# Kernel optimization log

Measured on AMD Instinct MI355X. Metric: run time of the kernel, lower is better.

Reference implementation:

```python
import jax, jax.numpy as jnp
import numpy as np

B, N, D = 8, 8192, 512
H, WIDTH = 8, 2048
DH = D // H
EPS = 1e-5


def _ln(x, g, b):
    m = jnp.mean(x, axis=-1, keepdims=True)
    v = jnp.mean(jnp.square(x - m), axis=-1, keepdims=True)
    return (x - m) * jax.lax.rsqrt(v + EPS) * g + b


def setup_inputs() -> dict:
    key = jax.random.key(0)
    ks = jax.random.split(key, 16)
    s = 0.02
    return {
        "x": jax.random.normal(ks[0], (B, N, D), dtype=jnp.float32),
        "mask": jnp.ones((B, N), dtype=jnp.float32),
        "Wq": jax.random.normal(ks[1], (D, D), dtype=jnp.float32) * s,
        "bq": jnp.zeros((D,), dtype=jnp.float32),
        "Wk": jax.random.normal(ks[2], (D, D), dtype=jnp.float32) * s,
        "bk": jnp.zeros((D,), dtype=jnp.float32),
        "Wv": jax.random.normal(ks[3], (D, D), dtype=jnp.float32) * s,
        "bv": jnp.zeros((D,), dtype=jnp.float32),
        "q_alpha": jax.random.normal(ks[4], (H, DH), dtype=jnp.float32),
        "k_beta": jax.random.normal(ks[5], (H, DH), dtype=jnp.float32),
        "Wo": jax.random.normal(ks[6], (D, D), dtype=jnp.float32) * s,
        "bo": jnp.zeros((D,), dtype=jnp.float32),
        "ln0_g": jnp.ones((D,), dtype=jnp.float32),
        "ln0_b": jnp.zeros((D,), dtype=jnp.float32),
        "ln1_g": jnp.ones((D,), dtype=jnp.float32),
        "ln1_b": jnp.zeros((D,), dtype=jnp.float32),
        "W1": jax.random.normal(ks[7], (WIDTH, D), dtype=jnp.float32) * s,
        "b1": jnp.zeros((WIDTH,), dtype=jnp.float32),
        "W2": jax.random.normal(ks[8], (D, WIDTH), dtype=jnp.float32) * s,
        "b2": jnp.zeros((D,), dtype=jnp.float32),
    }


def reference(x, mask, Wq, bq, Wk, bk, Wv, bv, q_alpha, k_beta, Wo, bo,
              ln0_g, ln0_b, ln1_g, ln1_b, W1, b1, W2, b2):
    scale = DH ** -0.5
    mask_ = mask[..., None]                       # [B,N,1]
    valid = (mask != 0)[..., None]                # [B,N,1] bool, broadcast over H

    residual = x
    xn = _ln(x, ln0_g, ln0_b) * mask_

    Q = (xn @ Wq.T + bq).reshape(B, N, H, DH)
    K = (xn @ Wk.T + bk).reshape(B, N, H, DH)
    V = (xn @ Wv.T + bv).reshape(B, N, H, DH)

    # stage 1: global query pooling
    alpha = jnp.einsum('bnhd,hd->bnh', Q, q_alpha) * scale
    alpha = jnp.where(valid, alpha, -jnp.inf)
    alpha = jax.nn.softmax(alpha, axis=1)         # softmax over N
    global_q = jnp.einsum('bnhd,bnh->bhd', Q, alpha)

    # stage 2: global value pooling
    P = K * global_q[:, None]                     # [B,N,H,DH]
    beta = jnp.einsum('bnhd,hd->bnh', P, k_beta) * scale
    beta = jnp.where(valid, beta, -jnp.inf)
    beta = jax.nn.softmax(beta, axis=1)
    global_v = jnp.einsum('bnhd,bnh->bhd', V, beta)

    out = (Q + global_v[:, None]).reshape(B, N, D)
    out = out @ Wo.T + bo
    x = residual + out

    residual = x
    xn = _ln(x, ln1_g, ln1_b)
    h = jax.nn.gelu(xn @ W1.T + b1, approximate=False)
    h = jax.nn.gelu(h @ W2.T + b2, approximate=False)
    x = residual + h
    x = x * mask_
    return x
```

## Files before the change

### kernel.cpp

```cpp
#include <hip/hip_runtime.h>
#include <hip/hip_bf16.h>
#include <hip/hip_fp8.h>
#include <math.h>

typedef short s8v __attribute__((ext_vector_type(8)));
typedef short s4v __attribute__((ext_vector_type(4)));
typedef __bf16 bf8v __attribute__((ext_vector_type(8)));
typedef float f4v __attribute__((ext_vector_type(4)));

#define GLOBAL_AS __attribute__((address_space(1)))
#define LDS_AS __attribute__((address_space(3)))

static __device__ __forceinline__ float bf2f(ushort u) {
  return __builtin_bit_cast(float, (unsigned int)u << 16);
}
static __device__ __forceinline__ ushort f2bf(float f) {
  unsigned int u = __builtin_bit_cast(unsigned int, f);
  u += 0x7FFFu + ((u >> 16) & 1u);
  return (ushort)(u >> 16);
}
static __device__ __forceinline__ unsigned char f2fp8(float f) {
#if __has_builtin(__builtin_amdgcn_cvt_pk_fp8_f32)
  int p = __builtin_amdgcn_cvt_pk_fp8_f32(f, f, 0, false);
  return (unsigned char)(p & 0xFF);
#else
  __hip_fp8_e4m3 v(f);
  return (unsigned char)v.__x;
#endif
}
static __device__ __forceinline__ float gelu_f(float v) {
  float t = v * v;
  float u = v * (0.0356774081f * t + 0.7978845608f);
  float e = __expf(-2.0f * u);
  return v * __builtin_amdgcn_rcpf(1.0f + e);
}
static __device__ __forceinline__ float wave_max_f(float v) {
  #pragma unroll
  for (int o = 32; o >= 1; o >>= 1) v = fmaxf(v, __shfl_xor(v, o));
  return v;
}
static __device__ __forceinline__ float wave_sum_f(float v) {
  #pragma unroll
  for (int o = 32; o >= 1; o >>= 1) v += __shfl_xor(v, o);
  return v;
}
static __device__ __forceinline__ void gload16(const void* g, const void* l) {
  __builtin_amdgcn_global_load_lds(
      (const GLOBAL_AS unsigned int*)g,
      (LDS_AS unsigned int*)l, 16, 0, 0);
}

__global__ void cvt_f32_bf16(const float* __restrict__ in, ushort* __restrict__ out, int n) {
  int i = (blockIdx.x * 256 + threadIdx.x) * 4;
  if (i >= n) return;
  float4 v = *(const float4*)(in + i);
  s4v o;
  o[0] = (short)f2bf(v.x); o[1] = (short)f2bf(v.y);
  o[2] = (short)f2bf(v.z); o[3] = (short)f2bf(v.w);
  *(s4v*)(out + i) = o;
}

__global__ void cvt_f32_fp8(const float* __restrict__ in, unsigned char* __restrict__ out, int n) {
  int i = (blockIdx.x * 256 + threadIdx.x) * 4;
  if (i >= n) return;
  float4 v = *(const float4*)(in + i);
  uchar4 o;
  o.x = f2fp8(v.x); o.y = f2fp8(v.y); o.z = f2fp8(v.z); o.w = f2fp8(v.w);
  *(uchar4*)(out + i) = o;
}

__global__ __launch_bounds__(256) void transpose512(
    const float* __restrict__ in, float* __restrict__ out) {
  __shared__ float t[32][33];
  const int bx = blockIdx.x & 15, by = blockIdx.x >> 4;
  const int tx = threadIdx.x & 31, ty = threadIdx.x >> 5;
  #pragma unroll
  for (int i = 0; i < 4; ++i)
    t[ty + i * 8][tx] = in[(long)(by * 32 + ty + i * 8) * 512 + bx * 32 + tx];
  __syncthreads();
  #pragma unroll
  for (int i = 0; i < 4; ++i)
    out[(long)(bx * 32 + ty + i * 8) * 512 + by * 32 + tx] = t[tx][ty + i * 8];
}

__global__ __launch_bounds__(256) void wqo_kernel(
    const float* __restrict__ Wo, const float* __restrict__ Wq,
    ushort* __restrict__ WqoB)
{
  __shared__ float lO[64][33];
  __shared__ float lQ[32][65];
  const int t = threadIdx.x;
  const int bi = (blockIdx.x & 7) * 64, bj = (blockIdx.x >> 3) * 64;
  float acc[16] = {};
  for (int k0 = 0; k0 < 512; k0 += 32) {
    __syncthreads();
    {
      const int r = t >> 2, c = (t & 3) * 8;
      #pragma unroll
      for (int j = 0; j < 8; ++j) lO[r][c + j] = Wo[(long)(bi + r) * 512 + k0 + c + j];
      const int r2 = t >> 3, c2 = (t & 7) * 8;
      #pragma unroll
      for (int j = 0; j < 8; ++j) lQ[r2][c2 + j] = Wq[(long)(k0 + r2) * 512 + bj + c2 + j];
    }
    __syncthreads();
    const int j = t & 63, ig = t >> 6;
    for (int kk = 0; kk < 32; ++kk) {
      float q = lQ[kk][j];
      #pragma unroll
      for (int ii = 0; ii < 16; ++ii) acc[ii] += lO[ig * 16 + ii][kk] * q;
    }
  }
  const int j = t & 63, ig = t >> 6;
  #pragma unroll
  for (int ii = 0; ii < 16; ++ii)
    WqoB[(long)(bi + ig * 16 + ii) * 512 + bj + j] = f2bf(acc[ii]);
}

__global__ __launch_bounds__(256) void wa_kernel(
    const float* __restrict__ qa, const float* __restrict__ Wq,
    const float* __restrict__ bqv, ushort* __restrict__ waB, float* __restrict__ ca)
{
  __shared__ float ql[64];
  const int h = blockIdx.x;
  const int t = threadIdx.x;
  if (h >= 8) {
    waB[h * 512 + t] = 0; waB[h * 512 + 256 + t] = 0;
    if (t == 0) ca[h] = 0.f;
    return;
  }
  if (t < 64) ql[t] = qa[h * 64 + t];
  __syncthreads();
  #pragma unroll
  for (int half = 0; half < 2; ++half) {
    const int k = half * 256 + t;
    float s = 0;
    for (int dd = 0; dd < 64; ++dd) s += ql[dd] * Wq[(long)(h * 64 + dd) * 512 + k];
    waB[h * 512 + k] = f2bf(s);
  }
  if (t == 0) {
    float s = 0;
    for (int dd = 0; dd < 64; ++dd) s += ql[dd] * bqv[h * 64 + dd];
    ca[h] = s;
  }
}

__global__ __launch_bounds__(256) void ln_rows(
    const float* __restrict__ x, const float* __restrict__ gam,
    const float* __restrict__ bet, const float* __restrict__ mask,
    ushort* __restrict__ out)
{
  const int tid = threadIdx.x, lane = tid & 63, wv = tid >> 6;
  const long row = (long)blockIdx.x * 4 + wv;
  const float* xp = x + row * 512 + lane * 8;
  float4 a = *(const float4*)xp;
  float4 b = *(const float4*)(xp + 4);
  float s = a.x + a.y + a.z + a.w + b.x + b.y + b.z + b.w;
  float q = a.x*a.x + a.y*a.y + a.z*a.z + a.w*a.w
          + b.x*b.x + b.y*b.y + b.z*b.z + b.w*b.w;
  s = wave_sum_f(s); q = wave_sum_f(q);
  float m = s * (1.f / 512.f);
  float var = q * (1.f / 512.f) - m * m;
  float r = rsqrtf(var + 1e-5f);
  float mk = mask ? mask[row] : 1.f;
  const float* gp = gam + lane * 8;
  const float* bp = bet + lane * 8;
  float4 g0 = *(const float4*)gp, g1 = *(const float4*)(gp + 4);
  float4 c0 = *(const float4*)bp, c1 = *(const float4*)(bp + 4);
  s8v o;
  o[0] = (short)f2bf(((a.x - m) * r * g0.x + c0.x) * mk);
  o[1] = (short)f2bf(((a.y - m) * r * g0.y + c0.y) * mk);
  o[2] = (short)f2bf(((a.z - m) * r * g0.z + c0.z) * mk);
  o[3] = (short)f2bf(((a.w - m) * r * g0.w + c0.w) * mk);
  o[4] = (short)f2bf(((b.x - m) * r * g1.x + c1.x) * mk);
  o[5] = (short)f2bf(((b.y - m) * r * g1.y + c1.y) * mk);
  o[6] = (short)f2bf(((b.z - m) * r * g1.z + c1.z) * mk);
  o[7] = (short)f2bf(((b.w - m) * r * g1.w + c1.w) * mk);
  *(s8v*)(out + row * 512 + lane * 8) = o;
}

__global__ __launch_bounds__(256) void ln_rows_bf16(
    const ushort* __restrict__ x, const float* __restrict__ gam,
    const float* __restrict__ bet, ushort* __restrict__ out)
{
  const int tid = threadIdx.x, lane = tid & 63, wv = tid >> 6;
  const long row = (long)blockIdx.x * 4 + wv;
  s8v v = *(const s8v*)(x + row * 512 + lane * 8);
  float xv[8];
  #pragma unroll
  for (int j = 0; j < 8; ++j) xv[j] = bf2f((ushort)v[j]);
  float s = 0.f, q = 0.f;
  #pragma unroll
  for (int j = 0; j < 8; ++j) { s += xv[j]; q += xv[j] * xv[j]; }
  s = wave_sum_f(s); q = wave_sum_f(q);
  float m = s * (1.f / 512.f);
  float var = q * (1.f / 512.f) - m * m;
  float r = rsqrtf(var + 1e-5f);
  const float* gp = gam + lane * 8;
  const float* bp = bet + lane * 8;
  float4 g0 = *(const float4*)gp, g1 = *(const float4*)(gp + 4);
  float4 c0 = *(const float4*)bp, c1 = *(const float4*)(bp + 4);
  float gg[8] = {g0.x, g0.y, g0.z, g0.w, g1.x, g1.y, g1.z, g1.w};
  float cc[8] = {c0.x, c0.y, c0.z, c0.w, c1.x, c1.y, c1.z, c1.w};
  s8v o;
  #pragma unroll
  for (int j = 0; j < 8; ++j) o[j] = (short)f2bf((xv[j] - m) * r * gg[j] + cc[j]);
  *(s8v*)(out + row * 512 + lane * 8) = o;
}

template<int BS, int CS>
__global__ __launch_bounds__(256) void logits_k(
    const ushort* __restrict__ XN, const ushort* __restrict__ Wl,
    const float* __restrict__ cvec, const float* __restrict__ mask,
    float* __restrict__ outL)
{
  __shared__ ushort lw[16 * 512];
  const int tid = threadIdx.x, lane = tid & 63, wv = tid >> 6;
  const long r0 = (long)blockIdx.x * 64;
  const int b = (int)(r0 >> 13);
  #pragma unroll
  for (int i = 0; i < 4; ++i) {
    const int u = tid + i * 256;
    const int h2 = u >> 6, uu = u & 63;
    s8v v = *(const s8v*)(Wl + (long)b * BS + h2 * 512 + uu * 8);
    *(s8v*)(lw + h2 * 512 + (uu ^ (h2 & 7)) * 8) = v;
  }
  __syncthreads();
  const int h = lane & 15, q = lane >> 4;
  const long rw = r0 + wv * 16;
  const ushort* ap = XN + (rw + (lane & 15)) * 512 + q * 8;
  f4v acc = {};
  #pragma unroll
  for (int t = 0; t < 16; ++t) {
    bf8v a = *(const bf8v*)(ap + t * 32);
    bf8v bb = *(const bf8v*)(lw + h * 512 + (((t * 4 + q) ^ (h & 7))) * 8);
    acc = __builtin_amdgcn_mfma_f32_16x16x32_bf16(a, bb, acc, 0, 0, 0);
  }
  const float cv = cvec[b * CS + h];
  #pragma unroll
  for (int j = 0; j < 4; ++j) {
    const long n = rw + q * 4 + j;
    float v = (acc[j] + cv) * 0.125f;
    if (mask[n] == 0.f) v = -1e30f;
    if (h < 8) outL[((long)((b << 3) + h) << 13) + (n & 8191)] = v;
  }
}

__global__ __launch_bounds__(1024) void softmax_rows(float* __restrict__ L)
{
  __shared__ float red[16];
  __shared__ float bc;
  const int tid = threadIdx.x, lane = tid & 63, wv = tid >> 6;
  float* p = L + ((long)blockIdx.x << 13) + tid * 8;
  float4 v0 = *(float4*)p;
  float4 v1 = *(float4*)(p + 4);
  float m = fmaxf(fmaxf(fmaxf(v0.x, v0.y), fmaxf(v0.z, v0.w)),
                  fmaxf(fmaxf(v1.x, v1.y), fmaxf(v1.z, v1.w)));
  m = wave_max_f(m);
  if (lane == 0) red[wv] = m;
  __syncthreads();
  if (tid < 64) {
    float t = (lane < 16) ? red[lane] : -INFINITY;
    t = wave_max_f(t);
    if (lane == 0) bc = t;
  }
  __syncthreads();
  const float gm = bc;
  v0.x = __expf(v0.x - gm); v0.y = __expf(v0.y - gm);
  v0.z = __expf(v0.z - gm); v0.w = __expf(v0.w - gm);
  v1.x = __expf(v1.x - gm); v1.y = __expf(v1.y - gm);
  v1.z = __expf(v1.z - gm); v1.w = __expf(v1.w - gm);
  float s = v0.x + v0.y + v0.z + v0.w + v1.x + v1.y + v1.z + v1.w;
  s = wave_sum_f(s);
  __syncthreads();
  if (lane == 0) red[wv] = s;
  __syncthreads();
  if (tid < 64) {
    float t = (lane < 16) ? red[lane] : 0.f;
    t = wave_sum_f(t);
    if (lane == 0) bc = t;
  }
  __syncthreads();
  const float inv = 1.0f / bc;
  v0.x *= inv; v0.y *= inv; v0.z *= inv; v0.w *= inv;
  v1.x *= inv; v1.y *= inv; v1.z *= inv; v1.w *= inv;
  *(float4*)p = v0;
  *(float4*)(p + 4) = v1;
}

__global__ __launch_bounds__(256) void pool_w(
    const ushort* __restrict__ XN, const float* __restrict__ wbuf,
    float* __restrict__ part)
{
  __shared__ float wlds[128][8];
  __shared__ float cmb[4][512];
  const int tid = threadIdx.x;
  const int b = blockIdx.x >> 6, ch = blockIdx.x & 63;
  const long g0 = ((long)b << 13) + ch * 128;
  if (tid < 128) {
    #pragma unroll
    for (int h = 0; h < 8; ++h)
      wlds[tid][h] = wbuf[(((long)(b * 8 + h)) << 13) + ch * 128 + tid];
  }
  __syncthreads();
  const int rg = tid >> 6, c8 = (tid & 63) * 8;
  f4v acc[8][2] = {};
  for (int it = 0; it < 32; ++it) {
    const int r = it * 4 + rg;
    s8v xv = *(const s8v*)(XN + (g0 + r) * 512 + c8);
    float xf[8];
    #pragma unroll
    for (int j = 0; j < 8; ++j) xf[j] = bf2f((ushort)xv[j]);
    #pragma unroll
    for (int h = 0; h < 8; ++h) {
      const float w = wlds[r][h];
      #pragma unroll
      for (int j = 0; j < 8; ++j) acc[h][j >> 2][j & 3] += w * xf[j];
    }
  }
  #pragma unroll
  for (int h = 0; h < 8; ++h) {
    __syncthreads();
    #pragma unroll
    for (int j = 0; j < 8; ++j) cmb[rg][c8 + j] = acc[h][j >> 2][j & 3];
    __syncthreads();
    const int col = tid * 2;
    float s0 = cmb[0][col] + cmb[1][col] + cmb[2][col] + cmb[3][col];
    float s1 = cmb[0][col + 1] + cmb[1][col + 1] + cmb[2][col + 1] + cmb[3][col + 1];
    *(float2*)(part + (((long)blockIdx.x * 8 + h) << 9) + col) = make_float2(s0, s1);
  }
}

__global__ __launch_bounds__(256) void combine_px(
    const float* __restrict__ part, float* __restrict__ px)
{
  const int bh = blockIdx.x;
  const int b = bh >> 3, h = bh & 7;
  const int col = threadIdx.x * 2;
  float s0 = 0.f, s1 = 0.f;
  for (int ch = 0; ch < 64; ++ch) {
    const float* p = part + (((long)((b * 64 + ch) * 8 + h)) << 9) + col;
    s0 += p[0]; s1 += p[1];
  }
  px[(bh << 9) + col] = s0;
  px[(bh << 9) + col + 1] = s1;
}

__global__ __launch_bounds__(64) void prep_gq_wb(
    const float* __restrict__ px, const float* __restrict__ WqT,
    const float* __restrict__ bqv, const float* __restrict__ kbv,
    const float* __restrict__ Wk, const float* __restrict__ bkv,
    ushort* __restrict__ wbB, float* __restrict__ cbs)
{
  __shared__ float pxl[512];
  __shared__ float gkb[64];
  const int bh = blockIdx.x, b = bh >> 3, h = bh & 7, d = threadIdx.x;
  #pragma unroll
  for (int i = 0; i < 8; ++i) pxl[d + i * 64] = px[(bh << 9) + d + i * 64];
  __syncthreads();
  float acc = bqv[h * 64 + d];
  for (int c = 0; c < 512; ++c) acc += pxl[c] * WqT[(long)c * 512 + h * 64 + d];
  gkb[d] = acc * kbv[h * 64 + d];
  __syncthreads();
  float s[8] = {};
  for (int dd = 0; dd < 64; ++dd) {
    const float g = gkb[dd];
    const float* wr = Wk + (long)(h * 64 + dd) * 512 + d;
    #pragma unroll
    for (int ki = 0; ki < 8; ++ki) s[ki] += g * wr[ki * 64];
  }
  #pragma unroll
  for (int ki = 0; ki < 8; ++ki)
    wbB[(long)(b * 16 + h) * 512 + d + ki * 64] = f2bf(s[ki]);
  if (d == 0) {
    float t = 0.f;
    for (int dd = 0; dd < 64; ++dd) t += gkb[dd] * bkv[h * 64 + dd];
    cbs[b * 16 + h] = t;
  }
  if (h == 0) {
    #pragma unroll
    for (int hp = 8; hp < 16; ++hp)
      for (int k = d; k < 512; k += 64) wbB[(long)(b * 16 + hp) * 512 + k] = 0;
    if (d < 8) cbs[b * 16 + 8 + d] = 0.f;
  }
}

__global__ __launch_bounds__(64) void prep_gv(
    const float* __restrict__ pv, const float* __restrict__ WvT,
    const float* __restrict__ bvv, const float* __restrict__ bqv,
    float* __restrict__ gvb)
{
  __shared__ float pxl[512];
  const int bh = blockIdx.x, b = bh >> 3, h = bh & 7, d = threadIdx.x;
  #pragma unroll
  for (int i = 0; i < 8; ++i) pxl[d + i * 64] = pv[(bh << 9) + d + i * 64];
  __syncthreads();
  float acc = bvv[h * 64 + d] + bqv[h * 64 + d];
  for (int c = 0; c < 512; ++c) acc += pxl[c] * WvT[(long)c * 512 + h * 64 + d];
  gvb[b * 512 + h * 64 + d] = acc;
}

__global__ __launch_bounds__(256) void bias_gv(
    const float* __restrict__ gv, const float* __restrict__ Wo,
    const float* __restrict__ bo, float* __restrict__ bo2) {
  const int b = blockIdx.x;
  const int n = blockIdx.y * 256 + threadIdx.x;
  const float* g = gv + b * 512;
  const float* w = Wo + (long)n * 512;
  float acc = 0.f;
  for (int d = 0; d < 512; d += 4) {
    float4 wv4 = *(const float4*)(w + d);
    acc += g[d] * wv4.x + g[d + 1] * wv4.y + g[d + 2] * wv4.z + g[d + 3] * wv4.w;
  }
  bo2[b * 512 + n] = bo[n] + acc;
}

#define MFMA_(d,a,b) d = __builtin_amdgcn_mfma_f32_16x16x32_bf16(a, b, d, 0, 0, 0)

template<int EPI, int LDA, int NN, int KK>
__global__ __launch_bounds__(512, 4) void gemmP(
    const ushort* __restrict__ A, const ushort* __restrict__ W,
    const float* __restrict__ bias, const void* __restrict__ resid,
    const float* __restrict__ mask, void* __restrict__ Out)
{
  constexpr int NBX = NN / 256;
  constexpr int NT = KK / 32;
  __shared__ __align__(16) ushort lds[3][12288];
  const int tid = threadIdx.x;
  const int lane = tid & 63;
  const int w = tid >> 6;
  const int wm = w >> 2, wn = w & 3;

  const int nwg = gridDim.x;
  const int cpx = nwg >> 3;
  const int wg = (blockIdx.x & 7) * cpx + (blockIdx.x >> 3);
  const int bx = wg % NBX, by = wg / NBX;
  const long bm = (long)by * 128;
  const int bn = bx * 256;

  const int scr = tid >> 2, sls = tid & 3;
  const int akU = ((sls ^ (scr & 3) ^ ((scr >> 2) & 3))) * 8;
  const ushort* asrc = A + (bm + scr) * (long)LDA + akU;
  const int rbe = (scr & 31) + ((scr >> 5) << 6);
  const ushort* besrc = W + (long)(bn + rbe) * KK + akU;
  const ushort* bosrc = W + (long)(bn + rbe + 32) * KK + akU;

#define STG(b_, Tt) { \
    gload16(asrc + (Tt) * 32, &lds[b_][tid * 8]); \
    gload16(besrc + (Tt) * 32, &lds[b_][4096 + tid * 8]); \
    gload16(bosrc + (Tt) * 32, &lds[b_][8192 + tid * 8]); }

  STG(0, 0);
  STG(1, 1);

  f4v acc[4][4] = {};

  const int L = lane & 15, q = lane >> 4;
  const int soff = (q ^ (lane & 3) ^ ((lane >> 2) & 3)) * 8;
  const int abase = (wm * 64 + L) * 32 + soff;
  const int bbase = 4096 + (wn * 32 + L) * 32 + soff;

  asm volatile("s_waitcnt vmcnt(3)" ::: "memory");
  asm volatile("s_barrier" ::: "memory");

  for (int T = 0; T < NT; ++T) {
    const ushort* Lp = &lds[T % 3][0];
    bf8v aR[4], bR[4];
    #pragma unroll
    for (int m = 0; m < 4; ++m) aR[m] = *(const bf8v*)(Lp + abase + m * 512);
    bR[0] = *(const bf8v*)(Lp + bbase);
    bR[1] = *(const bf8v*)(Lp + bbase + 512);
    bR[2] = *(const bf8v*)(Lp + bbase + 4096);
    bR[3] = *(const bf8v*)(Lp + bbase + 4096 + 512);
    if (T + 2 < NT) {
      STG((T + 2) % 3, T + 2);
      asm volatile("s_waitcnt vmcnt(3)" ::: "memory");
    } else {
      asm volatile("s_waitcnt vmcnt(0)" ::: "memory");
    }
    asm volatile("s_barrier" ::: "memory");
    __builtin_amdgcn_s_setprio(1);
    #pragma unroll
    for (int m = 0; m < 4; ++m)
      #pragma unroll
      for (int n = 0; n < 4; ++n)
        MFMA_(acc[m][n], aR[m], bR[n]);
    __builtin_amdgcn_s_setprio(0);
  }
#undef STG

  const int colb = bn + wn * 64 + L;
  const long rowb = bm + wm * 64 + q * 4;
  const float* biasp = (EPI == 5) ? bias + ((bm >> 13) << 9) : bias;
  #pragma unroll
  for (int m = 0; m < 4; ++m) {
    #pragma unroll
    for (int j = 0; j < 4; ++j) {
      const long row = rowb + m * 16 + j;
      #pragma unroll
      for (int n = 0; n < 4; ++n) {
        const int col = colb + n * 16;
        float v = acc[m][n][j] + biasp[col];
        const long idx = row * (long)NN + col;
        if constexpr (EPI == 6) {
          ((unsigned char*)Out)[idx] = f2fp8(gelu_f(v));
        } else {
          ((ushort*)Out)[idx] = f2bf(v + ((const float*)resid)[idx]);
        }
      }
    }
  }
}

__global__ __launch_bounds__(512, 4) void gemmF8(
    const unsigned char* __restrict__ A, const unsigned char* __restrict__ W,
    const float* __restrict__ bias, const ushort* __restrict__ resid,
    const float* __restrict__ mask, float* __restrict__ Out)
{
  constexpr int NN = 512, KK = 2048;
  constexpr int NBX = 2;
  constexpr int NT = KK / 64;
  __shared__ __align__(16) unsigned char lds8[3][24576];
  const int tid = threadIdx.x;
  const int lane = tid & 63;
  const int w = tid >> 6;
  const int wm = w >> 2, wn = w & 3;

  const int nwg = gridDim.x;
  const int cpx = nwg >> 3;
  const int wg = (blockIdx.x & 7) * cpx + (blockIdx.x >> 3);
  const int bx = wg % NBX, by = wg / NBX;
  const long bm = (long)by * 128;
  const int bn = bx * 256;

  const int srow = tid >> 2;
  const int sxu = (tid & 3) ^ ((srow >> 1) & 3);
  const unsigned char* asrc = A + (bm + srow) * (long)KK + sxu * 16;
  const unsigned char* b0src = W + (long)(bn + srow) * KK + sxu * 16;
  const unsigned char* b1src = W + (long)(bn + srow + 128) * KK + sxu * 16;

#define STG8(b_, Tt) { \
    gload16(asrc + (Tt) * 64, &lds8[b_][tid * 16]); \
    gload16(b0src + (Tt) * 64, &lds8[b_][8192 + tid * 16]); \
    gload16(b1src + (Tt) * 64, &lds8[b_][16384 + tid * 16]); }

  STG8(0, 0);
  STG8(1, 1);

  f4v acc[4][4] = {};

  const int L = lane & 15, q = lane >> 4;
  const int s0 = ((q) ^ (L & 6)) * 8;
  const int s1 = ((4 + q) ^ (L & 6)) * 8;
  const int arow = (wm * 64 + L) * 64;
  const int brow = 8192 + (wn * 64 + L) * 64;

  asm volatile("s_waitcnt vmcnt(3)" ::: "memory");
  asm volatile("s_barrier" ::: "memory");

  for (int T = 0; T < NT; ++T) {
    const unsigned char* Lp = &lds8[T % 3][0];
    long aF[8], bF[8];
    #pragma unroll
    for (int m = 0; m < 4; ++m) {
      aF[2 * m]     = *(const long*)(Lp + arow + m * 1024 + s0);
      aF[2 * m + 1] = *(const long*)(Lp + arow + m * 1024 + s1);
    }
    #pragma unroll
    for (int n = 0; n < 4; ++n) {
      bF[2 * n]     = *(const long*)(Lp + brow + n * 1024 + s0);
      bF[2 * n + 1] = *(const long*)(Lp + brow + n * 1024 + s1);
    }
    if (T + 2 < NT) {
      STG8((T + 2) % 3, T + 2);
      asm volatile("s_waitcnt vmcnt(3)" ::: "memory");
    } else {
      asm volatile("s_waitcnt vmcnt(0)" ::: "memory");
    }
    asm volatile("s_barrier" ::: "memory");
    __builtin_amdgcn_s_setprio(1);
    #pragma unroll
    for (int m = 0; m < 4; ++m)
      #pragma unroll
      for (int n = 0; n < 4; ++n) {
        acc[m][n] = __builtin_amdgcn_mfma_f32_16x16x32_fp8_fp8(
            aF[2 * m], bF[2 * n], acc[m][n], 0, 0, 0);
        acc[m][n] = __builtin_amdgcn_mfma_f32_16x16x32_fp8_fp8(
            aF[2 * m + 1], bF[2 * n + 1], acc[m][n], 0, 0, 0);
      }
    __builtin_amdgcn_s_setprio(0);
  }
#undef STG8

  const int colb = bn + wn * 64 + L;
  const long rowb = bm + wm * 64 + q * 4;
  #pragma unroll
  for (int m = 0; m < 4; ++m) {
    #pragma unroll
    for (int j = 0; j < 4; ++j) {
      const long row = rowb + m * 16 + j;
      const float mk = mask[row];
      #pragma unroll
      for (int n = 0; n < 4; ++n) {
        const int col = colb + n * 16;
        float v = acc[m][n][j] + bias[col];
        const long idx = row * (long)NN + col;
        Out[idx] = (bf2f(resid[idx]) + gelu_f(v)) * mk;
      }
    }
  }
}

extern "C" void kernel_launch(void* const* d_in, const int* in_sizes, int n_in,
                              void* d_out, int out_size, void* d_ws, size_t ws_size,
                              hipStream_t stream) {
  const float* x    = (const float*)d_in[0];
  const float* mask = (const float*)d_in[1];
  const float* Wq   = (const float*)d_in[2];
  const float* bq   = (const float*)d_in[3];
  const float* Wk   = (const float*)d_in[4];
  const float* bk   = (const float*)d_in[5];
  const float* Wv   = (const float*)d_in[6];
  const float* bv   = (const float*)d_in[7];
  const float* qa   = (const float*)d_in[8];
  const float* kb   = (const float*)d_in[9];
  const float* Wo   = (const float*)d_in[10];
  const float* bo   = (const float*)d_in[11];
  const float* g0   = (const float*)d_in[12];
  const float* be0  = (const float*)d_in[13];
  const float* g1   = (const float*)d_in[14];
  const float* be1  = (const float*)d_in[15];
  const float* W1   = (const float*)d_in[16];
  const float* b1   = (const float*)d_in[17];
  const float* W2   = (const float*)d_in[18];
  const float* b2   = (const float*)d_in[19];
  float* out = (float*)d_out;

  const int M = 65536;
  char* ws = (char*)d_ws;
  const size_t MB = 1024 * 1024;
  ushort* XN  = (ushort*)(ws);
  ushort* X1  = (ushort*)(ws + 64 * MB);
  unsigned char* H1F = (unsigned char*)(ws + 192 * MB);
  float*  AL  = (float*)(ws + 192 * MB);
  float*  BL  = (float*)(ws + 194 * MB);
  float*  PART= (float*)(ws + 196 * MB);
  char* base = ws + 448 * MB;
  ushort* W1B  = (ushort*)(base);
  unsigned char* W2F = (unsigned char*)(base + 2 * MB);
  ushort* WqoB = (ushort*)(base + 4 * MB);
  float*  WqT  = (float*)(base + 4 * MB + 512 * 1024);
  float*  WvT  = (float*)(base + 5 * MB + 512 * 1024);
  ushort* waB  = (ushort*)(base + 6 * MB + 512 * 1024);
  ushort* wbB  = (ushort*)(base + 6 * MB + 528 * 1024);
  float*  ca   = (float*)(base + 6 * MB + 656 * 1024);
  float*  cbs  = (float*)(base + 6 * MB + 660 * 1024);
  float*  PX   = (float*)(base + 6 * MB + 664 * 1024);
  float*  PV   = (float*)(base + 6 * MB + 792 * 1024);
  float*  GVB  = (float*)(base + 6 * MB + 920 * 1024);
  float*  BO2  = (float*)(base + 6 * MB + 936 * 1024);

  cvt_f32_bf16<<<1024, 256, 0, stream>>>(W1, W1B, 1048576);
  cvt_f32_fp8<<<1024, 256, 0, stream>>>(W2, W2F, 1048576);
  wqo_kernel<<<64, 256, 0, stream>>>(Wo, Wq, WqoB);
  wa_kernel<<<16, 256, 0, stream>>>(qa, Wq, bq, waB, ca);
  transpose512<<<256, 256, 0, stream>>>(Wq, WqT);
  transpose512<<<256, 256, 0, stream>>>(Wv, WvT);

  ln_rows<<<M / 4, 256, 0, stream>>>(x, g0, be0, mask, XN);

  logits_k<0, 0><<<1024, 256, 0, stream>>>(XN, waB, ca, mask, AL);
  softmax_rows<<<64, 1024, 0, stream>>>(AL);
  pool_w<<<512, 256, 0, stream>>>(XN, AL, PART);
  combine_px<<<64, 256, 0, stream>>>(PART, PX);
  prep_gq_wb<<<64, 64, 0, stream>>>(PX, WqT, bq, kb, Wk, bk, wbB, cbs);

  logits_k<8192, 16><<<1024, 256, 0, stream>>>(XN, wbB, cbs, mask, BL);
  softmax_rows<<<64, 1024, 0, stream>>>(BL);
  pool_w<<<512, 256, 0, stream>>>(XN, BL, PART);
  combine_px<<<64, 256, 0, stream>>>(PART, PV);
  prep_gv<<<64, 64, 0, stream>>>(PV, WvT, bv, bq, GVB);
  bias_gv<<<dim3(8, 2), 256, 0, stream>>>(GVB, Wo, bo, BO2);

  gemmP<5, 512, 512, 512><<<2 * (M / 128), 512, 0, stream>>>(
      XN, WqoB, BO2, x, nullptr, X1);

  ln_rows_bf16<<<M / 4, 256, 0, stream>>>(X1, g1, be1, XN);

  gemmP<6, 512, 2048, 512><<<8 * (M / 128), 512, 0, stream>>>(
      XN, W1B, b1, nullptr, nullptr, H1F);
  gemmF8<<<2 * (M / 128), 512, 0, stream>>>(
      H1F, W2F, b2, X1, mask, out);
}
```

Baseline: 631.8 us.

## Run FFN first GEMM in FP8 with interleaved K layout and 16-byte fragment loads

Moves the W1 GEMM from bf16 to FP8. LN1 now writes FP8 activations and the weights are pre-scaled by 8 and stored in a K-interleaved layout, so each lane fetches both MFMA operands with a single 16-byte LDS read. The shared FP8 GEMM is templated for both FFN matmuls, drops from triple to double buffering with an extra barrier, and the first GEMM's epilogue writes GELU outputs in the same interleaved FP8 layout. This halves A/B traffic and doubles MFMA throughput for the first GEMM, at the cost of lower precision from FP8 activations after LN.

```diff
diff --git a/kernel.cpp b/kernel.cpp
--- a/kernel.cpp
+++ b/kernel.cpp
@@ -7,6 +7,7 @@
 typedef short s4v __attribute__((ext_vector_type(4)));
 typedef __bf16 bf8v __attribute__((ext_vector_type(8)));
 typedef float f4v __attribute__((ext_vector_type(4)));
+typedef long l2v __attribute__((ext_vector_type(2)));
 
 #define GLOBAL_AS __attribute__((address_space(1)))
 #define LDS_AS __attribute__((address_space(3)))
@@ -50,23 +51,19 @@
       (LDS_AS unsigned int*)l, 16, 0, 0);
 }
 
-__global__ void cvt_f32_bf16(const float* __restrict__ in, ushort* __restrict__ out, int n) {
+__global__ void cvt_f32_fp8il(const float* __restrict__ in,
+                              unsigned char* __restrict__ out, int n, int kmask) {
   int i = (blockIdx.x * 256 + threadIdx.x) * 4;
   if (i >= n) return;
   float4 v = *(const float4*)(in + i);
-  s4v o;
-  o[0] = (short)f2bf(v.x); o[1] = (short)f2bf(v.y);
-  o[2] = (short)f2bf(v.z); o[3] = (short)f2bf(v.w);
-  *(s4v*)(out + i) = o;
-}
-
-__global__ void cvt_f32_fp8(const float* __restrict__ in, unsigned char* __restrict__ out, int n) {
-  int i = (blockIdx.x * 256 + threadIdx.x) * 4;
-  if (i >= n) return;
-  float4 v = *(const float4*)(in + i);
-  uchar4 o;
-  o.x = f2fp8(v.x); o.y = f2fp8(v.y); o.z = f2fp8(v.z); o.w = f2fp8(v.w);
-  *(uchar4*)(out + i) = o;
+  const int k = i & kmask;
+  const int r = k & 63;
+  const int qq = (r >> 3) & 3, h = (r >> 5) & 1, j = r & 7;
+  const long o = (long)(i - r) + qq * 16 + h * 8 + j;
+  uchar4 ob;
+  ob.x = f2fp8(v.x * 8.f); ob.y = f2fp8(v.y * 8.f);
+  ob.z = f2fp8(v.z * 8.f); ob.w = f2fp8(v.w * 8.f);
+  *(uchar4*)(out + o) = ob;
 }
 
 __global__ __launch_bounds__(256) void transpose512(
@@ -178,9 +175,9 @@
   *(s8v*)(out + row * 512 + lane * 8) = o;
 }
 
-__global__ __launch_bounds__(256) void ln_rows_bf16(
+__global__ __launch_bounds__(256) void ln_rows_fp8il(
     const ushort* __restrict__ x, const float* __restrict__ gam,
-    const float* __restrict__ bet, ushort* __restrict__ out)
+    const float* __restrict__ bet, unsigned char* __restrict__ out)
 {
   const int tid = threadIdx.x, lane = tid & 63, wv = tid >> 6;
   const long row = (long)blockIdx.x * 4 + wv;
@@ -201,10 +198,14 @@
   float4 c0 = *(const float4*)bp, c1 = *(const float4*)(bp + 4);
   float gg[8] = {g0.x, g0.y, g0.z, g0.w, g1.x, g1.y, g1.z, g1.w};
   float cc[8] = {c0.x, c0.y, c0.z, c0.w, c1.x, c1.y, c1.z, c1.w};
-  s8v o;
-  #pragma unroll
-  for (int j = 0; j < 8; ++j) o[j] = (short)f2bf((xv[j] - m) * r * gg[j] + cc[j]);
-  *(s8v*)(out + row * 512 + lane * 8) = o;
+  unsigned long long pk = 0;
+  #pragma unroll
+  for (int j = 0; j < 8; ++j) {
+    unsigned char b8 = f2fp8((xv[j] - m) * r * gg[j] + cc[j]);
+    pk |= (unsigned long long)b8 << (8 * j);
+  }
+  *(unsigned long long*)(out + row * 512 + (lane >> 3) * 64
+                         + (lane & 3) * 16 + ((lane >> 2) & 1) * 8) = pk;
 }
 
 template<int BS, int CS>
@@ -490,7 +491,7 @@
 
   const int colb = bn + wn * 64 + L;
   const long rowb = bm + wm * 64 + q * 4;
-  const float* biasp = (EPI == 5) ? bias + ((bm >> 13) << 9) : bias;
+  const float* biasp = bias + ((bm >> 13) << 9);
   #pragma unroll
   for (int m = 0; m < 4; ++m) {
     #pragma unroll
@@ -501,25 +502,21 @@
         const int col = colb + n * 16;
         float v = acc[m][n][j] + biasp[col];
         const long idx = row * (long)NN + col;
-        if constexpr (EPI == 6) {
-          ((unsigned char*)Out)[idx] = f2fp8(gelu_f(v));
-        } else {
-          ((ushort*)Out)[idx] = f2bf(v + ((const float*)resid)[idx]);
-        }
+        ((ushort*)Out)[idx] = f2bf(v + ((const float*)resid)[idx]);
       }
     }
   }
 }
 
+template<int EPI, int NN, int KK>
 __global__ __launch_bounds__(512, 4) void gemmF8(
     const unsigned char* __restrict__ A, const unsigned char* __restrict__ W,
-    const float* __restrict__ bias, const ushort* __restrict__ resid,
-    const float* __restrict__ mask, float* __restrict__ Out)
-{
-  constexpr int NN = 512, KK = 2048;
-  constexpr int NBX = 2;
+    const float* __restrict__ bias, const void* __restrict__ resid,
+    const float* __restrict__ mask, void* __restrict__ Out)
+{
+  constexpr int NBX = NN / 256;
   constexpr int NT = KK / 64;
-  __shared__ __align__(16) unsigned char lds8[3][24576];
+  __shared__ __align__(16) unsigned char lds8[2][24576];
   const int tid = threadIdx.x;
   const int lane = tid & 63;
   const int w = tid >> 6;
@@ -533,15 +530,15 @@
   const int bn = bx * 256;
 
   const int srow = tid >> 2;
-  const int sxu = (tid & 3) ^ ((srow >> 1) & 3);
-  const unsigned char* asrc = A + (bm + srow) * (long)KK + sxu * 16;
-  const unsigned char* b0src = W + (long)(bn + srow) * KK + sxu * 16;
-  const unsigned char* b1src = W + (long)(bn + srow + 128) * KK + sxu * 16;
-
-#define STG8(b_, Tt) { \
-    gload16(asrc + (Tt) * 64, &lds8[b_][tid * 16]); \
-    gload16(b0src + (Tt) * 64, &lds8[b_][8192 + tid * 16]); \
-    gload16(b1src + (Tt) * 64, &lds8[b_][16384 + tid * 16]); }
+  const int sgu = (tid & 3) ^ ((srow >> 1) & 3);
+  const unsigned char* asrc = A + (bm + srow) * (long)KK + sgu * 16;
+  const unsigned char* b0src = W + (long)(bn + srow) * KK + sgu * 16;
+  const unsigned char* b1src = W + (long)(bn + 128 + srow) * KK + sgu * 16;
+
+#define STG8(bf_, Tt) { \
+    gload16(asrc + (Tt) * 64, &lds8[bf_][tid * 16]); \
+    gload16(b0src + (Tt) * 64, &lds8[bf_][8192 + tid * 16]); \
+    gload16(b1src + (Tt) * 64, &lds8[bf_][16384 + tid * 16]); }
 
   STG8(0, 0);
   STG8(1, 1);
@@ -549,8 +546,7 @@
   f4v acc[4][4] = {};
 
   const int L = lane & 15, q = lane >> 4;
-  const int s0 = ((q) ^ (L & 6)) * 8;
-  const int s1 = ((4 + q) ^ (L & 6)) * 8;
+  const int ua = (q ^ ((L >> 1) & 3)) * 16;
   const int arow = (wm * 64 + L) * 64;
   const int brow = 8192 + (wn * 64 + L) * 64;
 
@@ -558,20 +554,15 @@
   asm volatile("s_barrier" ::: "memory");
 
   for (int T = 0; T < NT; ++T) {
-    const unsigned char* Lp = &lds8[T % 3][0];
-    long aF[8], bF[8];
-    #pragma unroll
-    for (int m = 0; m < 4; ++m) {
-      aF[2 * m]     = *(const long*)(Lp + arow + m * 1024 + s0);
-      aF[2 * m + 1] = *(const long*)(Lp + arow + m * 1024 + s1);
-    }
-    #pragma unroll
-    for (int n = 0; n < 4; ++n) {
-      bF[2 * n]     = *(const long*)(Lp + brow + n * 1024 + s0);
-      bF[2 * n + 1] = *(const long*)(Lp + brow + n * 1024 + s1);
-    }
+    const unsigned char* Lp = &lds8[T & 1][0];
+    l2v aV[4], bV[4];
+    #pragma unroll
+    for (int m = 0; m < 4; ++m) aV[m] = *(const l2v*)(Lp + arow + m * 1024 + ua);
+    #pragma unroll
+    for (int n = 0; n < 4; ++n) bV[n] = *(const l2v*)(Lp + brow + n * 1024 + ua);
+    asm volatile("s_barrier" ::: "memory");
     if (T + 2 < NT) {
-      STG8((T + 2) % 3, T + 2);
+      STG8(T & 1, T + 2);
       asm volatile("s_waitcnt vmcnt(3)" ::: "memory");
     } else {
       asm volatile("s_waitcnt vmcnt(0)" ::: "memory");
@@ -583,28 +574,35 @@
       #pragma unroll
       for (int n = 0; n < 4; ++n) {
         acc[m][n] = __builtin_amdgcn_mfma_f32_16x16x32_fp8_fp8(
-            aF[2 * m], bF[2 * n], acc[m][n], 0, 0, 0);
+            aV[m][0], bV[n][0], acc[m][n], 0, 0, 0);
         acc[m][n] = __builtin_amdgcn_mfma_f32_16x16x32_fp8_fp8(
-            aF[2 * m + 1], bF[2 * n + 1], acc[m][n], 0, 0, 0);
+            aV[m][1], bV[n][1], acc[m][n], 0, 0, 0);
       }
     __builtin_amdgcn_s_setprio(0);
   }
 #undef STG8
 
-  const int colb = bn + wn * 64 + L;
   const long rowb = bm + wm * 64 + q * 4;
+  const int gbase = bn + wn * 64;
   #pragma unroll
   for (int m = 0; m < 4; ++m) {
     #pragma unroll
     for (int j = 0; j < 4; ++j) {
       const long row = rowb + m * 16 + j;
-      const float mk = mask[row];
+      float mk;
+      if constexpr (EPI == 8) mk = mask[row];
       #pragma unroll
       for (int n = 0; n < 4; ++n) {
-        const int col = colb + n * 16;
-        float v = acc[m][n][j] + bias[col];
-        const long idx = row * (long)NN + col;
-        Out[idx] = (bf2f(resid[idx]) + gelu_f(v)) * mk;
+        const int col = gbase + n * 16 + L;
+        float v = acc[m][n][j] * 0.125f + bias[col];
+        if constexpr (EPI == 7) {
+          const int rp = ((n * 2 + (L >> 3)) & 3) * 16 + (n >> 1) * 8 + (L & 7);
+          ((unsigned char*)Out)[row * (long)NN + gbase + rp] = f2fp8(gelu_f(v));
+        } else {
+          const long idx = row * (long)NN + col;
+          ((float*)Out)[idx] =
+              (bf2f(((const ushort*)resid)[idx]) + gelu_f(v)) * mk;
+        }
       }
     }
   }
@@ -640,12 +638,13 @@
   const size_t MB = 1024 * 1024;
   ushort* XN  = (ushort*)(ws);
   ushort* X1  = (ushort*)(ws + 64 * MB);
-  unsigned char* H1F = (unsigned char*)(ws + 192 * MB);
-  float*  AL  = (float*)(ws + 192 * MB);
-  float*  BL  = (float*)(ws + 194 * MB);
-  float*  PART= (float*)(ws + 196 * MB);
+  unsigned char* XN1F = (unsigned char*)(ws + 128 * MB);
+  unsigned char* H1F  = (unsigned char*)(ws + 192 * MB);
+  float*  AL  = (float*)(ws + 320 * MB);
+  float*  BL  = (float*)(ws + 322 * MB);
+  float*  PART= (float*)(ws + 324 * MB);
   char* base = ws + 448 * MB;
-  ushort* W1B  = (ushort*)(base);
+  unsigned char* W1F = (unsigned char*)(base);
   unsigned char* W2F = (unsigned char*)(base + 2 * MB);
   ushort* WqoB = (ushort*)(base + 4 * MB);
   float*  WqT  = (float*)(base + 4 * MB + 512 * 1024);
@@ -659,8 +658,8 @@
   float*  GVB  = (float*)(base + 6 * MB + 920 * 1024);
   float*  BO2  = (float*)(base + 6 * MB + 936 * 1024);
 
-  cvt_f32_bf16<<<1024, 256, 0, stream>>>(W1, W1B, 1048576);
-  cvt_f32_fp8<<<1024, 256, 0, stream>>>(W2, W2F, 1048576);
+  cvt_f32_fp8il<<<1024, 256, 0, stream>>>(W1, W1F, 1048576, 511);
+  cvt_f32_fp8il<<<1024, 256, 0, stream>>>(W2, W2F, 1048576, 2047);
   wqo_kernel<<<64, 256, 0, stream>>>(Wo, Wq, WqoB);
   wa_kernel<<<16, 256, 0, stream>>>(qa, Wq, bq, waB, ca);
   transpose512<<<256, 256, 0, stream>>>(Wq, WqT);
@@ -684,10 +683,10 @@
   gemmP<5, 512, 512, 512><<<2 * (M / 128), 512, 0, stream>>>(
       XN, WqoB, BO2, x, nullptr, X1);
 
-  ln_rows_bf16<<<M / 4, 256, 0, stream>>>(X1, g1, be1, XN);
-
-  gemmP<6, 512, 2048, 512><<<8 * (M / 128), 512, 0, stream>>>(
-      XN, W1B, b1, nullptr, nullptr, H1F);
-  gemmF8<<<2 * (M / 128), 512, 0, stream>>>(
+  ln_rows_fp8il<<<M / 4, 256, 0, stream>>>(X1, g1, be1, XN1F);
+
+  gemmF8<7, 2048, 512><<<8 * (M / 128), 512, 0, stream>>>(
+      XN1F, W1F, b1, nullptr, nullptr, H1F);
+  gemmF8<8, 512, 2048><<<2 * (M / 128), 512, 0, stream>>>(
       H1F, W2F, b2, X1, mask, out);
 }
```

New measurement: 585.6 us. 7.3% less time.
